# Optimization experiments

Hardware: AMD Instinct MI355X
Metric: run time of the kernel (lower is better)

## Reference

```python
import jax, jax.numpy as jnp
import numpy as np

B, S, DIM, H, HD = 2, 2048, 512, 8, 64
VD = DIM // H  # 64
QK = H * HD


def setup_inputs() -> dict:
    key = jax.random.key(0)
    k1, k2, k3, k4, k5 = jax.random.split(key, 5)
    x = jax.random.normal(k1, (B, S, DIM), dtype=jnp.float32)
    mask = jax.random.bernoulli(k2, 0.5, (B, S))
    # per-position rotation matrices, scaled to keep activations O(1)
    rotator = jax.random.normal(k3, (B, S, HD, HD), dtype=jnp.float32) / np.sqrt(HD)
    # torch Linear weights: [out_features, in_features], no bias
    W_trans = jax.random.normal(k4, (2 * QK + DIM, DIM), dtype=jnp.float32) / np.sqrt(DIM)
    W_o = jax.random.normal(k5, (DIM, DIM), dtype=jnp.float32) / np.sqrt(DIM)
    return {"x": x, "mask": mask, "rotator": rotator, "W_trans": W_trans, "W_o": W_o}


def _taylor_attention(qs, ks, vs, mask):
    # 2nd-order Taylor approximation of exp for softmax weights
    # qs/ks: [B,S,H,HD], vs: [B,S,H,VD], mask: [B,S] key mask
    scores = jnp.einsum('bqhd,bkhd->bhqk', qs, ks) / np.sqrt(HD)
    w = 1.0 + scores + 0.5 * scores * scores
    w = jnp.where(mask[:, None, None, :], w, 0.0)
    w = w / jnp.sum(w, axis=-1, keepdims=True)
    out = jnp.einsum('bhqk,bkhd->bqhd', w, vs)
    return out.reshape(out.shape[0], out.shape[1], -1)  # [B,S,DIM]


def reference(x, mask, rotator, W_trans, W_o):
    t = x @ W_trans.T  # [B,S,2*QK+DIM]
    qs = t[..., :QK].reshape(B, S, H, HD)
    ks = t[..., QK:2 * QK].reshape(B, S, H, HD)
    vs = t[..., 2 * QK:].reshape(B, S, H, VD)
    sel = mask[..., None, None]
    qs = jnp.where(sel, jnp.einsum('bsij,bshj->bshi', rotator, qs), qs)
    ks = jnp.where(sel, jnp.einsum('bsij,bshj->bshi', rotator, ks), ks)
    out = _taylor_attention(qs, ks, vs, mask)
    return out @ W_o.T
```

## Files before the change

kernel.cpp:

```cpp
#include <hip/hip_runtime.h>
#include <hip/hip_bf16.h>

#define B_    2
#define S_    2048
#define DIM_  512
#define H_    8
#define HD_   64
#define TOUT_ 1536
#define ROWS_ (B_ * S_)

typedef unsigned short ushort_t;
typedef __attribute__((ext_vector_type(8))) __bf16 bf16x8;
typedef __attribute__((ext_vector_type(4))) float floatx4;

#define AS_GLB __attribute__((address_space(1)))
#define AS_LDS __attribute__((address_space(3)))

__device__ __forceinline__ unsigned short f2bfu(float f) {
    unsigned u = __float_as_uint(f);
    unsigned r = (u + 0x7fffu + ((u >> 16) & 1u)) >> 16;
    return (unsigned short)r;
}
__device__ __forceinline__ bf16x8 cvt8(const float* p) {
    float4 a = *reinterpret_cast<const float4*>(p);
    float4 b = *reinterpret_cast<const float4*>(p + 4);
    ushort_t o[8] = {f2bfu(a.x), f2bfu(a.y), f2bfu(a.z), f2bfu(a.w),
                     f2bfu(b.x), f2bfu(b.y), f2bfu(b.z), f2bfu(b.w)};
    return *reinterpret_cast<bf16x8*>(o);
}

#define XN4_  (ROWS_ * DIM_ / 4)
#define WTN4_ (TOUT_ * DIM_ / 4)
#define WON4_ (DIM_ * DIM_ / 4)
#define CASTBLKS_ ((XN4_ + WTN4_ + WON4_) / 256)
__global__ __launch_bounds__(256) void prep_inputs(const float* __restrict__ x,
                                                   const float* __restrict__ wt,
                                                   const float* __restrict__ wo,
                                                   const unsigned char* __restrict__ mb,
                                                   ushort_t* __restrict__ xb,
                                                   ushort_t* __restrict__ wtb,
                                                   ushort_t* __restrict__ wob,
                                                   int* __restrict__ wm) {
    if (blockIdx.x >= CASTBLKS_) {
        __shared__ int s_bf, s_f, s_u8;
        int tid = threadIdx.x;
        if (tid == 0) { s_bf = 0; s_f = 0; s_u8 = 0; }
        __syncthreads();
        int cbf = 0, cf = 0, cu8 = 0;
        for (int i = tid; i < 4096; i += 256) {
            unsigned char v = mb[i];
            if (v == 0x3F || v == 0x80) {
                cf++;
                if ((i & 3) == 1) cbf++;
            } else if (v != 0 && (i & 3) != 0) {
                cu8++;
            }
        }
        atomicAdd(&s_bf, cbf); atomicAdd(&s_f, cf); atomicAdd(&s_u8, cu8);
        __syncthreads();
        int cls = (s_bf > 0) ? 2 : (s_f > 0) ? 3 : (s_u8 > 0) ? 0 : 1;
        for (int i = tid; i < ROWS_; i += 256) {
            int v;
            if (cls == 0)      v = (mb[i] != 0);
            else if (cls == 1) v = (reinterpret_cast<const int*>(mb)[i] != 0);
            else if (cls == 2) v = ((reinterpret_cast<const unsigned short*>(mb)[i] & 0x7fffu) != 0);
            else               v = ((reinterpret_cast<const unsigned int*>(mb)[i] & 0x7fffffffu) != 0);
            wm[i] = v;
        }
        return;
    }
    int i = blockIdx.x * 256 + threadIdx.x;
    const float* s; ushort_t* d; int off;
    if (i < XN4_)              { s = x;  d = xb;  off = i; }
    else if (i < XN4_ + WTN4_) { s = wt; d = wtb; off = i - XN4_; }
    else                       { s = wo; d = wob; off = i - XN4_ - WTN4_; }
    float4 v = reinterpret_cast<const float4*>(s)[off];
    ushort_t o[4] = {f2bfu(v.x), f2bfu(v.y), f2bfu(v.z), f2bfu(v.w)};
    reinterpret_cast<uint2*>(d)[off] = *reinterpret_cast<uint2*>(o);
}

template <int TM, int N, int K, bool OUT_BF16>
__global__ __launch_bounds__(256) void mfma_gemm_bt(const ushort_t* __restrict__ A,
                                                    const ushort_t* __restrict__ Bm,
                                                    void* __restrict__ Cout) {
    constexpr int FM = (TM + 31) / 32;
    __shared__ __align__(16) ushort_t As[TM * 64];
    __shared__ __align__(16) ushort_t Bs[128 * 64];
    int tid = threadIdx.x;
    int lane = tid & 63;
    int wv = tid >> 6;
    int wm = wv >> 1, wn = wv & 1;
    int quad = lane >> 4;
    int mrow = lane & 15;
    int bx = blockIdx.x;
    int by = blockIdx.y;

    floatx4 acc[FM][4];
#pragma unroll
    for (int i = 0; i < FM; i++)
#pragma unroll
        for (int j = 0; j < 4; j++) acc[i][j] = (floatx4){0.f, 0.f, 0.f, 0.f};

    for (int k0 = 0; k0 < K; k0 += 64) {
#pragma unroll
        for (int t = 0; t < TM / 32; t++) {
            int p = (wv * (TM / 32) + t) * 64 + lane;
            int row = p >> 3, cp = p & 7;
            int gc = cp ^ (row & 7);
            const ushort_t* ga = A + (size_t)(by * TM + row) * K + k0 + gc * 8;
            __builtin_amdgcn_global_load_lds((const AS_GLB unsigned int*)ga,
                                             (AS_LDS unsigned int*)&As[(size_t)(wv * (TM / 32) + t) * 64 * 8],
                                             16, 0, 0);
        }
#pragma unroll
        for (int t = 0; t < 4; t++) {
            int p = (wv * 4 + t) * 64 + lane;
            int row = p >> 3, cp = p & 7;
            int gc = cp ^ (row & 7);
            const ushort_t* gb = Bm + (size_t)(bx * 128 + row) * K + k0 + gc * 8;
            __builtin_amdgcn_global_load_lds((const AS_GLB unsigned int*)gb,
                                             (AS_LDS unsigned int*)&Bs[(size_t)(wv * 4 + t) * 64 * 8],
                                             16, 0, 0);
        }
        __syncthreads();
#pragma unroll
        for (int ks = 0; ks < 64; ks += 32) {
            int c = (ks >> 3) + quad;
            bf16x8 af[FM], bf[4];
#pragma unroll
            for (int i = 0; i < FM; i++) {
                int row = wm * (TM / 2) + i * 16 + mrow;
                int pos = row * 8 + (c ^ (row & 7));
                af[i] = *reinterpret_cast<const bf16x8*>(&As[pos * 8]);
            }
#pragma unroll
            for (int j = 0; j < 4; j++) {
                int row = wn * 64 + j * 16 + mrow;
                int pos = row * 8 + (c ^ (row & 7));
                bf[j] = *reinterpret_cast<const bf16x8*>(&Bs[pos * 8]);
            }
#pragma unroll
            for (int i = 0; i < FM; i++)
#pragma unroll
                for (int j = 0; j < 4; j++)
                    acc[i][j] = __builtin_amdgcn_mfma_f32_16x16x32_bf16(af[i], bf[j], acc[i][j], 0, 0, 0);
        }
        __syncthreads();
    }

    int col0 = bx * 128 + wn * 64 + mrow;
    int row0 = by * TM + wm * (TM / 2) + quad * 4;
    if constexpr (OUT_BF16) {
        ushort_t* C = reinterpret_cast<ushort_t*>(Cout);
#pragma unroll
        for (int i = 0; i < FM; i++)
#pragma unroll
            for (int j = 0; j < 4; j++)
#pragma unroll
                for (int r = 0; r < 4; r++)
                    C[(size_t)(row0 + i * 16 + r) * N + col0 + j * 16] = f2bfu(acc[i][j][r]);
    } else {
        float* C = reinterpret_cast<float*>(Cout);
#pragma unroll
        for (int i = 0; i < FM; i++)
#pragma unroll
            for (int j = 0; j < 4; j++)
#pragma unroll
                for (int r = 0; r < 4; r++)
                    C[(size_t)(row0 + i * 16 + r) * N + col0 + j * 16] = acc[i][j][r];
    }
}

__global__ __launch_bounds__(256) void rot_qk_mfma(const ushort_t* __restrict__ t,
                                                   const float* __restrict__ rotG,
                                                   const int* __restrict__ wm,
                                                   ushort_t* __restrict__ Qb,
                                                   ushort_t* __restrict__ Kb) {
    int lane = threadIdx.x & 63;
    int wv = threadIdx.x >> 6;
    int row = blockIdx.x * 4 + wv;
    int b = row >> 11, s = row & 2047;
    int lm = lane & 15, quad = lane >> 4;
    const ushort_t* trow = t + (size_t)row * TOUT_;
    int kb = s >> 4, l = s & 15;

    if (wm[row]) {
        bf16x8 af[2];
#pragma unroll
        for (int kc = 0; kc < 2; kc++)
            af[kc] = *reinterpret_cast<const bf16x8*>(trow + lm * 64 + kc * 32 + quad * 8);

        const float* R = rotG + (size_t)row * 4096;
        floatx4 dacc[4];
#pragma unroll
        for (int nb = 0; nb < 4; nb++) dacc[nb] = (floatx4){0.f, 0.f, 0.f, 0.f};
#pragma unroll
        for (int nb = 0; nb < 4; nb++)
#pragma unroll
            for (int kc = 0; kc < 2; kc++) {
                bf16x8 bfr = cvt8(R + (size_t)(nb * 16 + lm) * 64 + kc * 32 + quad * 8);
                dacc[nb] = __builtin_amdgcn_mfma_f32_16x16x32_bf16(af[kc], bfr, dacc[nb], 0, 0, 0);
            }
#pragma unroll
        for (int nb = 0; nb < 4; nb++)
#pragma unroll
            for (int r = 0; r < 4; r++) {
                int vec = quad * 4 + r;
                int hh = vec & 7;
                ushort_t v = f2bfu(dacc[nb][r]);
                if (vec >= 8) {
                    int c = nb * 2 + (lm >> 3), e = lm & 7;
                    Kb[(((size_t)(b * 8 + hh) * 128 + kb) * 8 + c) * 128 + l * 8 + e] = v;
                } else {
                    Qb[((size_t)(b * 8 + hh) * 2048 + s) * 64 + nb * 16 + lm] = v;
                }
            }
    } else {
#pragma unroll
        for (int nb = 0; nb < 4; nb++)
#pragma unroll
            for (int r = 0; r < 4; r++) {
                int vec = quad * 4 + r;
                int hh = vec & 7;
                ushort_t v = trow[vec * 64 + nb * 16 + lm];
                if (vec >= 8) {
                    int c = nb * 2 + (lm >> 3), e = lm & 7;
                    Kb[(((size_t)(b * 8 + hh) * 128 + kb) * 8 + c) * 128 + l * 8 + e] = v;
                } else {
                    Qb[((size_t)(b * 8 + hh) * 2048 + s) * 64 + nb * 16 + lm] = v;
                }
            }
    }
}

__global__ __launch_bounds__(256) void prep_vt(const ushort_t* __restrict__ t,
                                               const int* __restrict__ wm,
                                               ushort_t* __restrict__ VtF,
                                               ushort_t* __restrict__ MrowG) {
    __shared__ ushort_t tile[64][72];
    __shared__ ushort_t umask[64];
    int st = blockIdx.x;
    int bh = blockIdx.y;
    int b = bh >> 3, h = bh & 7;
    int tid = threadIdx.x;
    if (tid < 64) umask[tid] = wm[b * 2048 + st * 64 + tid] ? 0xFFFFu : 0u;
#pragma unroll
    for (int i = 0; i < 2; i++) {
        int q = i * 256 + tid;
        int r = q >> 3, c8 = (q & 7) * 8;
        uint4 v = *reinterpret_cast<const uint4*>(
            t + (size_t)(b * 2048 + st * 64 + r) * TOUT_ + 1024 + h * 64 + c8);
        *reinterpret_cast<uint4*>(&tile[r][c8]) = v;
    }
    __syncthreads();
    if (tid < 32) {
        int sl = tid * 2;
        unsigned m0 = umask[sl]     ? 0x3F80u : 0u;
        unsigned m1 = umask[sl + 1] ? 0x3F80u : 0u;
        *reinterpret_cast<unsigned int*>(MrowG + (size_t)bh * 2048 + st * 64 + sl) = m0 | (m1 << 16);
    }
#pragma unroll
    for (int it = 0; it < 2; it++) {
        int idx = tid + it * 256;
        int d = idx & 63;
        int chunk = idx >> 6;
        ushort_t o[8];
#pragma unroll
        for (int e = 0; e < 8; e++)
            o[e] = (ushort_t)(tile[chunk * 8 + e][d] & umask[chunk * 8 + e]);
        *reinterpret_cast<uint4*>(
            VtF + ((((size_t)bh * 32 + st) * 8 + chunk) * 64 + d) * 8) = *reinterpret_cast<const uint4*>(o);
    }
}

__global__ __launch_bounds__(256) void tmha_attn_mfma(const ushort_t* __restrict__ Qb,
                                                      const ushort_t* __restrict__ KbF,
                                                      const ushort_t* __restrict__ VtF,
                                                      const ushort_t* __restrict__ MrowG,
                                                      ushort_t* __restrict__ attnAb) {
    __shared__ __align__(16) ushort_t Ps[512 * 8];
    int tid = threadIdx.x;
    int lane = tid & 63;
    int wv = tid >> 6;
    int lm = lane & 15;
    int quad = lane >> 4;

    int bid = blockIdx.x;
    int w = ((bid & 7) << 6) | (bid >> 3);
    int qt = w & 31;
    int bh = w >> 5;
    int b = bh >> 3, h = bh & 7;

    const ushort_t* Kf = KbF + (size_t)bh * 128 * 1024;
    const ushort_t* Vf = VtF + (size_t)bh * 32 * 8 * 64 * 8;
    const ushort_t* Mr = MrowG + (size_t)bh * 2048;

    bf16x8 qf[2];
    {
        const ushort_t* qp = Qb + ((size_t)bh * 2048 + qt * 64 + wv * 16 + lm) * 64 + quad * 8;
        qf[0] = *reinterpret_cast<const bf16x8*>(qp);
        qf[1] = *reinterpret_cast<const bf16x8*>(qp + 32);
    }

    bf16x8 vzero;
    *reinterpret_cast<uint4*>(&vzero) = (uint4){0u, 0u, 0u, 0u};

    floatx4 oacc[5];
#pragma unroll
    for (int j = 0; j < 5; j++) oacc[j] = (floatx4){0.f, 0.f, 0.f, 0.f};

    bf16x8 kr[4][2], vr[4][2], mvb[2];
    auto loadK = [&](int kt) {
        int kb = kt >> 4;
#pragma unroll
        for (int j = 0; j < 4; j++)
#pragma unroll
            for (int kc = 0; kc < 2; kc++)
                kr[j][kc] = *reinterpret_cast<const bf16x8*>(
                    Kf + (((size_t)(kb + j) * 8 + kc * 4 + quad) * 16 + lm) * 8);
    };
    auto loadV = [&](int kt) {
        int st = kt >> 6;
#pragma unroll
        for (int j = 0; j < 4; j++)
#pragma unroll
            for (int kc = 0; kc < 2; kc++)
                vr[j][kc] = *reinterpret_cast<const bf16x8*>(
                    Vf + (((size_t)st * 8 + kc * 4 + quad) * 64 + j * 16 + lm) * 8);
    };
    auto loadM = [&](int kt) {
#pragma unroll
        for (int kc = 0; kc < 2; kc++)
            mvb[kc] = *reinterpret_cast<const bf16x8*>(Mr + kt + (kc * 4 + quad) * 8);
    };

    loadK(0); loadV(0); loadM(0);
#pragma unroll 1
    for (int tt = 0; tt < 32; tt++) {
        int kt = tt * 64;
        int ktn = (tt == 31) ? 0 : kt + 64;

        floatx4 sacc[4];
#pragma unroll
        for (int j = 0; j < 4; j++) sacc[j] = (floatx4){0.f, 0.f, 0.f, 0.f};
        __builtin_amdgcn_s_setprio(1);
#pragma unroll
        for (int j = 0; j < 4; j++)
#pragma unroll
            for (int kc = 0; kc < 2; kc++)
                sacc[j] = __builtin_amdgcn_mfma_f32_16x16x32_bf16(qf[kc], kr[j][kc], sacc[j], 0, 0, 0);
        __builtin_amdgcn_s_setprio(0);

        loadK(ktn);

#pragma unroll
        for (int j = 0; j < 4; j++)
#pragma unroll
            for (int r = 0; r < 4; r++) {
                float s = sacc[j][r];
                float wgt = fmaf(s, fmaf(s, 0.0078125f, 0.125f), 1.0f);
                int m = wv * 16 + quad * 4 + r;
                int col = j * 16 + lm;
                int cw = col >> 3;
                int pos = m * 8 + (cw ^ (m & 7));
                Ps[pos * 8 + (col & 7)] = f2bfu(wgt);
            }
        asm volatile("s_waitcnt lgkmcnt(0)" ::: "memory");
        __builtin_amdgcn_sched_barrier(0);

        int qrow_l = wv * 16 + lm;
        bf16x8 pa[2];
#pragma unroll
        for (int kc = 0; kc < 2; kc++) {
            int c = kc * 4 + quad;
            int ppos = qrow_l * 8 + (c ^ (qrow_l & 7));
            pa[kc] = *reinterpret_cast<const bf16x8*>(&Ps[ppos * 8]);
        }
        __builtin_amdgcn_s_setprio(1);
#pragma unroll
        for (int j = 0; j < 4; j++)
#pragma unroll
            for (int kc = 0; kc < 2; kc++)
                oacc[j] = __builtin_amdgcn_mfma_f32_16x16x32_bf16(pa[kc], vr[j][kc], oacc[j], 0, 0, 0);
#pragma unroll
        for (int kc = 0; kc < 2; kc++) {
            bf16x8 vb = (lm == 0) ? mvb[kc] : vzero;
            oacc[4] = __builtin_amdgcn_mfma_f32_16x16x32_bf16(pa[kc], vb, oacc[4], 0, 0, 0);
        }
        __builtin_amdgcn_s_setprio(0);

        loadV(ktn); loadM(ktn);
    }

    float inv[4];
#pragma unroll
    for (int r = 0; r < 4; r++) {
        float dn = __shfl(oacc[4][r], lane & 48);
        inv[r] = 1.0f / dn;
    }
#pragma unroll
    for (int j = 0; j < 4; j++)
#pragma unroll
        for (int r = 0; r < 4; r++) {
            int qrow = b * 2048 + qt * 64 + wv * 16 + quad * 4 + r;
            attnAb[(size_t)qrow * DIM_ + h * 64 + j * 16 + lm] = f2bfu(oacc[j][r] * inv[r]);
        }
}

extern "C" void kernel_launch(void* const* d_in, const int* in_sizes, int n_in,
                              void* d_out, int out_size, void* d_ws, size_t ws_size,
                              hipStream_t stream) {
    (void)in_sizes; (void)n_in; (void)out_size; (void)ws_size;
    const float* x    = (const float*)d_in[0];
    const void*  mask = d_in[1];
    const float* rot  = (const float*)d_in[2];
    const float* Wt   = (const float*)d_in[3];
    const float* Wo   = (const float*)d_in[4];

    char* ws = (char*)d_ws;
    int* wmask       = (int*)(ws + 64);
    ushort_t* t      = (ushort_t*)(ws + 32768);
    ushort_t* Xb     = (ushort_t*)(ws + 25198592);
    ushort_t* Wtb    = (ushort_t*)(ws + 29392896);
    ushort_t* Wob    = (ushort_t*)(ws + 30965760);
    ushort_t* Qb     = (ushort_t*)(ws + 31490048);
    ushort_t* Kb     = (ushort_t*)(ws + 35684352);
    ushort_t* VtF    = (ushort_t*)(ws + 39878656);
    ushort_t* MrowG  = (ushort_t*)(ws + 44072960);
    ushort_t* attnAb = (ushort_t*)(ws + 44138496);

    prep_inputs<<<CASTBLKS_ + 1, 256, 0, stream>>>(x, Wt, Wo, (const unsigned char*)mask,
                                                   Xb, Wtb, Wob, wmask);

    {
        dim3 grid(TOUT_ / 128, ROWS_ / 64);
        mfma_gemm_bt<64, TOUT_, DIM_, true><<<grid, 256, 0, stream>>>(Xb, Wtb, (void*)t);
    }

    rot_qk_mfma<<<ROWS_ / 4, 256, 0, stream>>>(t, rot, wmask, Qb, Kb);

    {
        dim3 grid(32, 16);
        prep_vt<<<grid, 256, 0, stream>>>(t, wmask, VtF, MrowG);
    }

    tmha_attn_mfma<<<512, 256, 0, stream>>>(Qb, Kb, VtF, MrowG, attnAb);

    {
        dim3 grid(DIM_ / 128, ROWS_ / 32);
        mfma_gemm_bt<32, DIM_, DIM_, false><<<grid, 256, 0, stream>>>(attnAb, Wob, d_out);
    }
}
```

Measured before the change: 197.7 us.

## Compute transposed scores to keep P in registers, drop LDS round-trip

Swaps the MFMA operand order so the score tile comes out transposed (keys along rows), letting each lane pack its Taylor weights straight into a bf16x8 A-operand for the PV MFMA without staging through shared memory. The V pre-layout is rewritten to match that key ordering, and the mask-sum column is folded into V as a fifth 16-wide block so the denominator comes from the same loads. This removes the LDS write, the lgkmcnt wait and the LDS read per tile, plus the separate mask buffer. In exchange the V buffer is larger and more VGPRs hold the extra V block.

```diff
diff --git a/kernel.cpp b/kernel.cpp
--- a/kernel.cpp
+++ b/kernel.cpp
@@ -235,8 +235,7 @@
 
 __global__ __launch_bounds__(256) void prep_vt(const ushort_t* __restrict__ t,
                                                const int* __restrict__ wm,
-                                               ushort_t* __restrict__ VtF,
-                                               ushort_t* __restrict__ MrowG) {
+                                               ushort_t* __restrict__ VtF) {
     __shared__ ushort_t tile[64][72];
     __shared__ ushort_t umask[64];
     int st = blockIdx.x;
@@ -253,32 +252,40 @@
         *reinterpret_cast<uint4*>(&tile[r][c8]) = v;
     }
     __syncthreads();
-    if (tid < 32) {
-        int sl = tid * 2;
-        unsigned m0 = umask[sl]     ? 0x3F80u : 0u;
-        unsigned m1 = umask[sl + 1] ? 0x3F80u : 0u;
-        *reinterpret_cast<unsigned int*>(MrowG + (size_t)bh * 2048 + st * 64 + sl) = m0 | (m1 << 16);
-    }
-#pragma unroll
-    for (int it = 0; it < 2; it++) {
-        int idx = tid + it * 256;
-        int d = idx & 63;
-        int chunk = idx >> 6;
-        ushort_t o[8];
-#pragma unroll
-        for (int e = 0; e < 8; e++)
-            o[e] = (ushort_t)(tile[chunk * 8 + e][d] & umask[chunk * 8 + e]);
-        *reinterpret_cast<uint4*>(
-            VtF + ((((size_t)bh * 32 + st) * 8 + chunk) * 64 + d) * 8) = *reinterpret_cast<const uint4*>(o);
+    {
+        int dn = tid >> 6, quad = (tid >> 4) & 3, lm = tid & 15;
+#pragma unroll
+        for (int jj = 0; jj < 2; jj++) {
+            ushort_t o[8];
+#pragma unroll
+            for (int e = 0; e < 8; e++) {
+                int key = jj * 32 + ((e >> 2) << 4) + quad * 4 + (e & 3);
+                o[e] = (ushort_t)(tile[key][dn * 16 + lm] & umask[key]);
+            }
+            size_t base = (((((size_t)(bh * 32 + st) * 5 + dn) * 2 + jj) * 4 + quad) * 16 + lm) * 8;
+            *reinterpret_cast<uint4*>(VtF + base) = *reinterpret_cast<const uint4*>(o);
+        }
+    }
+    if (tid < 64) {
+        int quad = tid >> 4, lm = tid & 15;
+#pragma unroll
+        for (int jj = 0; jj < 2; jj++) {
+            ushort_t o[8];
+#pragma unroll
+            for (int e = 0; e < 8; e++) {
+                int key = jj * 32 + ((e >> 2) << 4) + quad * 4 + (e & 3);
+                o[e] = (lm == 0) ? (umask[key] ? (ushort_t)0x3F80u : (ushort_t)0u) : (ushort_t)0u;
+            }
+            size_t base = (((((size_t)(bh * 32 + st) * 5 + 4) * 2 + jj) * 4 + quad) * 16 + lm) * 8;
+            *reinterpret_cast<uint4*>(VtF + base) = *reinterpret_cast<const uint4*>(o);
+        }
     }
 }
 
 __global__ __launch_bounds__(256) void tmha_attn_mfma(const ushort_t* __restrict__ Qb,
                                                       const ushort_t* __restrict__ KbF,
                                                       const ushort_t* __restrict__ VtF,
-                                                      const ushort_t* __restrict__ MrowG,
                                                       ushort_t* __restrict__ attnAb) {
-    __shared__ __align__(16) ushort_t Ps[512 * 8];
     int tid = threadIdx.x;
     int lane = tid & 63;
     int wv = tid >> 6;
@@ -292,8 +299,7 @@
     int b = bh >> 3, h = bh & 7;
 
     const ushort_t* Kf = KbF + (size_t)bh * 128 * 1024;
-    const ushort_t* Vf = VtF + (size_t)bh * 32 * 8 * 64 * 8;
-    const ushort_t* Mr = MrowG + (size_t)bh * 2048;
+    const ushort_t* Vf = VtF + (size_t)bh * 163840;
 
     bf16x8 qf[2];
     {
@@ -302,14 +308,13 @@
         qf[1] = *reinterpret_cast<const bf16x8*>(qp + 32);
     }
 
-    bf16x8 vzero;
-    *reinterpret_cast<uint4*>(&vzero) = (uint4){0u, 0u, 0u, 0u};
-
+    floatx4 zero4 = (floatx4){0.f, 0.f, 0.f, 0.f};
     floatx4 oacc[5];
 #pragma unroll
-    for (int j = 0; j < 5; j++) oacc[j] = (floatx4){0.f, 0.f, 0.f, 0.f};
-
-    bf16x8 kr[4][2], vr[4][2], mvb[2];
+    for (int j = 0; j < 5; j++) oacc[j] = zero4;
+
+    bf16x8 kr[4][2];
+    bf16x8 vr[5][2];
     auto loadK = [&](int kt) {
         int kb = kt >> 4;
 #pragma unroll
@@ -320,76 +325,54 @@
                     Kf + (((size_t)(kb + j) * 8 + kc * 4 + quad) * 16 + lm) * 8);
     };
     auto loadV = [&](int kt) {
-        int st = kt >> 6;
-#pragma unroll
-        for (int j = 0; j < 4; j++)
-#pragma unroll
-            for (int kc = 0; kc < 2; kc++)
-                vr[j][kc] = *reinterpret_cast<const bf16x8*>(
-                    Vf + (((size_t)st * 8 + kc * 4 + quad) * 64 + j * 16 + lm) * 8);
+        const ushort_t* p = Vf + (size_t)(kt >> 6) * 5120 + quad * 128 + lm * 8;
+#pragma unroll
+        for (int dn = 0; dn < 5; dn++)
+#pragma unroll
+            for (int jj = 0; jj < 2; jj++)
+                vr[dn][jj] = *reinterpret_cast<const bf16x8*>(p + dn * 1024 + jj * 512);
     };
-    auto loadM = [&](int kt) {
-#pragma unroll
-        for (int kc = 0; kc < 2; kc++)
-            mvb[kc] = *reinterpret_cast<const bf16x8*>(Mr + kt + (kc * 4 + quad) * 8);
-    };
-
-    loadK(0); loadV(0); loadM(0);
+
+    loadK(0); loadV(0);
 #pragma unroll 1
     for (int tt = 0; tt < 32; tt++) {
-        int kt = tt * 64;
-        int ktn = (tt == 31) ? 0 : kt + 64;
+        int ktn = (tt == 31) ? 0 : (tt + 1) * 64;
 
         floatx4 sacc[4];
-#pragma unroll
-        for (int j = 0; j < 4; j++) sacc[j] = (floatx4){0.f, 0.f, 0.f, 0.f};
         __builtin_amdgcn_s_setprio(1);
 #pragma unroll
-        for (int j = 0; j < 4; j++)
-#pragma unroll
-            for (int kc = 0; kc < 2; kc++)
-                sacc[j] = __builtin_amdgcn_mfma_f32_16x16x32_bf16(qf[kc], kr[j][kc], sacc[j], 0, 0, 0);
+        for (int j = 0; j < 4; j++) {
+            sacc[j] = __builtin_amdgcn_mfma_f32_16x16x32_bf16(kr[j][0], qf[0], zero4, 0, 0, 0);
+            sacc[j] = __builtin_amdgcn_mfma_f32_16x16x32_bf16(kr[j][1], qf[1], sacc[j], 0, 0, 0);
+        }
         __builtin_amdgcn_s_setprio(0);
 
         loadK(ktn);
 
-#pragma unroll
-        for (int j = 0; j < 4; j++)
-#pragma unroll
-            for (int r = 0; r < 4; r++) {
-                float s = sacc[j][r];
-                float wgt = fmaf(s, fmaf(s, 0.0078125f, 0.125f), 1.0f);
-                int m = wv * 16 + quad * 4 + r;
-                int col = j * 16 + lm;
-                int cw = col >> 3;
-                int pos = m * 8 + (cw ^ (m & 7));
-                Ps[pos * 8 + (col & 7)] = f2bfu(wgt);
-            }
-        asm volatile("s_waitcnt lgkmcnt(0)" ::: "memory");
-        __builtin_amdgcn_sched_barrier(0);
-
-        int qrow_l = wv * 16 + lm;
-        bf16x8 pa[2];
-#pragma unroll
-        for (int kc = 0; kc < 2; kc++) {
-            int c = kc * 4 + quad;
-            int ppos = qrow_l * 8 + (c ^ (qrow_l & 7));
-            pa[kc] = *reinterpret_cast<const bf16x8*>(&Ps[ppos * 8]);
-        }
+        bf16x8 pa8[2];
+#pragma unroll
+        for (int jj = 0; jj < 2; jj++) {
+            ushort_t o[8];
+#pragma unroll
+            for (int half = 0; half < 2; half++)
+#pragma unroll
+                for (int r = 0; r < 4; r++) {
+                    float s = sacc[2 * jj + half][r];
+                    float wgt = fmaf(s, fmaf(s, 0.0078125f, 0.125f), 1.0f);
+                    o[half * 4 + r] = f2bfu(wgt);
+                }
+            pa8[jj] = *reinterpret_cast<bf16x8*>(o);
+        }
+
         __builtin_amdgcn_s_setprio(1);
 #pragma unroll
-        for (int j = 0; j < 4; j++)
-#pragma unroll
-            for (int kc = 0; kc < 2; kc++)
-                oacc[j] = __builtin_amdgcn_mfma_f32_16x16x32_bf16(pa[kc], vr[j][kc], oacc[j], 0, 0, 0);
-#pragma unroll
-        for (int kc = 0; kc < 2; kc++) {
-            bf16x8 vb = (lm == 0) ? mvb[kc] : vzero;
-            oacc[4] = __builtin_amdgcn_mfma_f32_16x16x32_bf16(pa[kc], vb, oacc[4], 0, 0, 0);
-        }
+        for (int jj = 0; jj < 2; jj++)
+#pragma unroll
+            for (int dn = 0; dn < 5; dn++)
+                oacc[dn] = __builtin_amdgcn_mfma_f32_16x16x32_bf16(pa8[jj], vr[dn][jj], oacc[dn], 0, 0, 0);
         __builtin_amdgcn_s_setprio(0);
 
-        loadV(ktn); loadM(ktn);
+        loadV(ktn);
     }
 
     float inv[4];
@@ -399,11 +382,11 @@
         inv[r] = 1.0f / dn;
     }
 #pragma unroll
-    for (int j = 0; j < 4; j++)
+    for (int dn = 0; dn < 4; dn++)
 #pragma unroll
         for (int r = 0; r < 4; r++) {
             int qrow = b * 2048 + qt * 64 + wv * 16 + quad * 4 + r;
-            attnAb[(size_t)qrow * DIM_ + h * 64 + j * 16 + lm] = f2bfu(oacc[j][r] * inv[r]);
+            attnAb[(size_t)qrow * DIM_ + h * 64 + dn * 16 + lm] = f2bfu(oacc[dn][r] * inv[r]);
         }
 }
 
@@ -420,14 +403,13 @@
     char* ws = (char*)d_ws;
     int* wmask       = (int*)(ws + 64);
     ushort_t* t      = (ushort_t*)(ws + 32768);
-    ushort_t* Xb     = (ushort_t*)(ws + 25198592);
-    ushort_t* Wtb    = (ushort_t*)(ws + 29392896);
-    ushort_t* Wob    = (ushort_t*)(ws + 30965760);
-    ushort_t* Qb     = (ushort_t*)(ws + 31490048);
-    ushort_t* Kb     = (ushort_t*)(ws + 35684352);
-    ushort_t* VtF    = (ushort_t*)(ws + 39878656);
-    ushort_t* MrowG  = (ushort_t*)(ws + 44072960);
-    ushort_t* attnAb = (ushort_t*)(ws + 44138496);
+    ushort_t* Xb     = (ushort_t*)(ws + 12615680);
+    ushort_t* Wtb    = (ushort_t*)(ws + 16809984);
+    ushort_t* Wob    = (ushort_t*)(ws + 18382848);
+    ushort_t* Qb     = (ushort_t*)(ws + 18907136);
+    ushort_t* Kb     = (ushort_t*)(ws + 23101440);
+    ushort_t* VtF    = (ushort_t*)(ws + 27295744);
+    ushort_t* attnAb = (ushort_t*)(ws + 32538624);
 
     prep_inputs<<<CASTBLKS_ + 1, 256, 0, stream>>>(x, Wt, Wo, (const unsigned char*)mask,
                                                    Xb, Wtb, Wob, wmask);
@@ -441,10 +423,10 @@
 
     {
         dim3 grid(32, 16);
-        prep_vt<<<grid, 256, 0, stream>>>(t, wmask, VtF, MrowG);
-    }
-
-    tmha_attn_mfma<<<512, 256, 0, stream>>>(Qb, Kb, VtF, MrowG, attnAb);
+        prep_vt<<<grid, 256, 0, stream>>>(t, wmask, VtF);
+    }
+
+    tmha_attn_mfma<<<512, 256, 0, stream>>>(Qb, Kb, VtF, attnAb);
 
     {
         dim3 grid(DIM_ / 128, ROWS_ / 32);
```

Measured after the change: 195.2 us. No clear change (-1.3%).
